# Kernel optimization log

Measured on AMD Instinct MI355X. Metric: run time of the kernel, lower is better.

The kernel has to match this reference:

```python
import jax, jax.numpy as jnp
import numpy as np

B, S, D = 4, 2048, 2048
H, KVH = 16, 4
HD = D // H            # 128
N_REP = H // KVH       # 4
SCALE = HD ** -0.5


def setup_inputs() -> dict:
    key = jax.random.key(0)
    ks = jax.random.split(key, 10)
    w = 0.02
    x = jax.random.normal(ks[0], (B, S, D), jnp.float32)
    # Linear weights stored as [in, out] (y = x @ W + b, equivalent to torch Linear)
    Wq = jax.random.normal(ks[1], (D, D), jnp.float32) * w
    bq = jnp.zeros((D,), jnp.float32)
    Wk = jax.random.normal(ks[2], (D, KVH * HD), jnp.float32) * w
    bk = jnp.zeros((KVH * HD,), jnp.float32)
    Wv = jax.random.normal(ks[3], (D, KVH * HD), jnp.float32) * w
    bv = jnp.zeros((KVH * HD,), jnp.float32)
    Wo = jax.random.normal(ks[4], (D, D), jnp.float32) * w
    bo = jnp.zeros((D,), jnp.float32)
    # RoPE tables: freqs_cis is [max_seq_len, head_dim//2] complex -> cos/sin
    inv_freq = 1.0 / (10000.0 ** (jnp.arange(0, HD, 2, dtype=jnp.float32) / HD))  # [HD//2]
    t = jnp.arange(S, dtype=jnp.float32)
    ang = jnp.outer(t, inv_freq)                     # [S, HD//2]
    freqs_cos = jnp.cos(ang)
    freqs_sin = jnp.sin(ang)
    # causal additive mask [1,1,S,S]
    neg = jnp.float32(-1e9)
    mask = jnp.where(jnp.triu(jnp.ones((S, S), bool), k=1), neg, 0.0)[None, None]
    return {"x": x, "Wq": Wq, "bq": bq, "Wk": Wk, "bk": bk, "Wv": Wv, "bv": bv,
            "Wo": Wo, "bo": bo, "freqs_cos": freqs_cos, "freqs_sin": freqs_sin,
            "mask": mask, "start_pos": 0}


def _apply_rope(q, k, cos, sin):
    # q: [B,S,H,HD], k: [B,S,KVH,HD]; interleaved complex pairs on last dim
    def rot(t):
        tr = t.reshape(*t.shape[:-1], HD // 2, 2)
        xr, xi = tr[..., 0], tr[..., 1]
        c = cos[None, :, None, :]
        s = sin[None, :, None, :]
        yr = xr * c - xi * s
        yi = xr * s + xi * c
        return jnp.stack([yr, yi], axis=-1).reshape(t.shape)
    return rot(q), rot(k)


def reference(x, Wq, bq, Wk, bk, Wv, bv, Wo, bo, freqs_cos, freqs_sin, mask, start_pos):
    Bx, Sx, _ = x.shape
    q = (x @ Wq + bq).reshape(Bx, Sx, H, HD)
    k = (x @ Wk + bk).reshape(Bx, Sx, KVH, HD)
    v = (x @ Wv + bv).reshape(Bx, Sx, KVH, HD)
    q, k = _apply_rope(q, k, freqs_cos, freqs_sin)
    # start_pos = 0 prefill: cache write-then-read is identity, so use k, v directly
    q = q.transpose(0, 2, 1, 3)                      # [B,H,S,HD]
    k = k.transpose(0, 2, 1, 3)                      # [B,KVH,S,HD]
    v = v.transpose(0, 2, 1, 3)
    k = jnp.repeat(k, N_REP, axis=1)                 # repeat_kv -> [B,H,S,HD]
    v = jnp.repeat(v, N_REP, axis=1)
    scores = jnp.einsum("bhsd,bhtd->bhst", q, k) * SCALE + mask
    w = jax.nn.softmax(scores, axis=-1)              # dropout p=0 -> identity
    out = jnp.einsum("bhst,bhtd->bhsd", w, v)
    out = out.transpose(0, 2, 1, 3).reshape(Bx, Sx, D)
    return out @ Wo + bo
```

## Files before the change

kernel.cpp:

```cpp
#include <hip/hip_runtime.h>

typedef unsigned short u16t;
typedef __bf16 bf16x8 __attribute__((ext_vector_type(8)));
typedef float f32x4 __attribute__((ext_vector_type(4)));
typedef float f32x16 __attribute__((ext_vector_type(16)));
typedef unsigned short ushort4_t __attribute__((ext_vector_type(4)));
typedef unsigned short ushort8_t __attribute__((ext_vector_type(8)));

#define B_    4
#define S_    2048
#define D_    2048
#define H_    16
#define KVH_  4
#define HD_   128
#define KDIM  2048
#define SCALE_ 0.08838834764831845f

__device__ __forceinline__ u16t f2bf(float f){
    unsigned u; __builtin_memcpy(&u, &f, 4);
    u += 0x7fffu + ((u >> 16) & 1u);
    return (u16t)(u >> 16);
}
__device__ __forceinline__ void glds16(const u16t* g, u16t* l){
    __builtin_amdgcn_global_load_lds((const __attribute__((address_space(1))) void*)g,
                                     (__attribute__((address_space(3))) void*)l, 16, 0, 0);
}
__device__ __forceinline__ void wg_barrier_lgkm(){
    __builtin_amdgcn_sched_barrier(0);
    asm volatile("s_waitcnt lgkmcnt(0)" ::: "memory");
    __builtin_amdgcn_s_barrier();
    __builtin_amdgcn_sched_barrier(0);
}
__device__ __forceinline__ unsigned cvt_pk_bf16(float lo, float hi){
    unsigned r;
    asm("v_cvt_pk_bf16_f32 %0, %1, %2" : "=v"(r) : "v"(lo), "v"(hi));
    return r;
}
__device__ __forceinline__ void permlane32_swap(unsigned &a, unsigned &b){
    asm volatile("v_permlane32_swap_b32 %0, %1" : "+v"(a), "+v"(b));
}

__global__ void f32_to_bf16(const float* __restrict__ in, u16t* __restrict__ out)
{
    int i = (blockIdx.x * 256 + threadIdx.x) * 4;
    float4 v = *(const float4*)(in + i);
    ushort4_t p;
    p[0] = f2bf(v.x); p[1] = f2bf(v.y); p[2] = f2bf(v.z); p[3] = f2bf(v.w);
    *(ushort4_t*)(out + i) = p;
}

__global__ void transpose_f32_bf16(const float* __restrict__ W, u16t* __restrict__ Wt,
                                   int Ncols, int Krows)
{
    __shared__ u16t tile[32][33];
    int tx = threadIdx.x, ty = threadIdx.y;
    int n = blockIdx.x * 32 + tx, k = blockIdx.y * 32 + ty;
    tile[ty][tx] = f2bf(W[(size_t)k * Ncols + n]);
    __syncthreads();
    int nn = blockIdx.x * 32 + ty, kk = blockIdx.y * 32 + tx;
    Wt[(size_t)nn * Krows + kk] = tile[tx][ty];
}

#define GEMM_PROLOGUE_AND_KLOOP                                                   \
    __shared__ u16t As[128 * 32];                                                 \
    __shared__ u16t Bs[128 * 32];                                                 \
    const int tid  = threadIdx.x;                                                 \
    const int lane = tid & 63, w = tid >> 6;                                      \
    const int wr = (w >> 1) * 64, wc = (w & 1) * 64;                              \
    const int lr = lane & 15, quad = lane >> 4;                                   \
    const int m0 = blockIdx.y * 128, n0 = blockIdx.x * 128;                       \
    f32x4 acc[4][4];                                                              \
    _Pragma("unroll")                                                             \
    for (int r = 0; r < 4; r++)                                                   \
        _Pragma("unroll")                                                         \
        for (int c = 0; c < 4; c++) acc[r][c] = (f32x4){0.f, 0.f, 0.f, 0.f};      \
    for (int k0 = 0; k0 < KDIM; k0 += 32) {                                       \
        __syncthreads();                                                          \
        _Pragma("unroll")                                                         \
        for (int cc = 0; cc < 2; cc++) {                                          \
            int slot = tid + cc * 256;                                            \
            int row = slot >> 2, ko = (slot & 3) * 8;                             \
            glds16(A  + (size_t)(m0 + row) * KDIM + k0 + ko, As + slot * 8);      \
            glds16(Bt + (size_t)(n0 + row) * KDIM + k0 + ko, Bs + slot * 8);      \
        }                                                                         \
        __syncthreads();                                                          \
        bf16x8 a[4], b[4];                                                        \
        _Pragma("unroll")                                                         \
        for (int r = 0; r < 4; r++)                                               \
            a[r] = *(const bf16x8*)(As + (wr + r * 16 + lr) * 32 + quad * 8);     \
        _Pragma("unroll")                                                         \
        for (int c = 0; c < 4; c++)                                               \
            b[c] = *(const bf16x8*)(Bs + (wc + c * 16 + lr) * 32 + quad * 8);     \
        _Pragma("unroll")                                                         \
        for (int r = 0; r < 4; r++)                                               \
            _Pragma("unroll")                                                     \
            for (int c = 0; c < 4; c++)                                           \
                acc[r][c] = __builtin_amdgcn_mfma_f32_16x16x32_bf16(a[r], b[c], acc[r][c], 0, 0, 0); \
    }

__global__ void gemm_o(const u16t* __restrict__ A, const u16t* __restrict__ Bt,
                       const float* __restrict__ bias, float* __restrict__ out)
{
    GEMM_PROLOGUE_AND_KLOOP
#pragma unroll
    for (int r = 0; r < 4; r++) {
#pragma unroll
        for (int c = 0; c < 4; c++) {
            int n = n0 + wc + c * 16 + lr;
            float bval = bias[n];
#pragma unroll
            for (int g = 0; g < 4; g++) {
                int m = m0 + wr + r * 16 + quad * 4 + g;
                out[(size_t)m * D_ + n] = acc[r][c][g] + bval;
            }
        }
    }
}

__global__ void gemm_qkv(const u16t* __restrict__ A, const u16t* __restrict__ Bt,
                         const float* __restrict__ bq, const float* __restrict__ bk,
                         const float* __restrict__ bv,
                         u16t* __restrict__ q_t, u16t* __restrict__ k_t,
                         u16t* __restrict__ v_t,
                         const float* __restrict__ fc, const float* __restrict__ fs)
{
    GEMM_PROLOGUE_AND_KLOOP
    const int region = (blockIdx.x < 16) ? 0 : ((blockIdx.x < 20) ? 1 : 2);
#pragma unroll
    for (int r = 0; r < 4; r++) {
#pragma unroll
        for (int c = 0; c < 4; c++) {
            int n = n0 + wc + c * 16 + lr;
            if (region == 0) {
                float bval = bq[n];
                int hh = n >> 7, d = n & 127, i2 = d >> 1;
#pragma unroll
                for (int g = 0; g < 4; g++) {
                    int m = m0 + wr + r * 16 + quad * 4 + g;
                    int bb = m >> 11, s = m & (S_ - 1);
                    float v = acc[r][c][g] + bval;
                    float p = __shfl_xor(v, 1);
                    float cf = fc[s * 64 + i2], sf = fs[s * 64 + i2];
                    float o = (d & 1) ? (p * sf + v * cf) : (v * cf - p * sf);
                    q_t[(((size_t)bb * H_ + hh) * S_ + s) * HD_ + d] = f2bf(o);
                }
            } else if (region == 1) {
                int nk = n - 2048;
                float bval = bk[nk];
                int hh = nk >> 7, d = nk & 127, i2 = d >> 1;
#pragma unroll
                for (int g = 0; g < 4; g++) {
                    int m = m0 + wr + r * 16 + quad * 4 + g;
                    int bb = m >> 11, s = m & (S_ - 1);
                    float v = acc[r][c][g] + bval;
                    float p = __shfl_xor(v, 1);
                    float cf = fc[s * 64 + i2], sf = fs[s * 64 + i2];
                    float o = (d & 1) ? (p * sf + v * cf) : (v * cf - p * sf);
                    k_t[(((size_t)bb * KVH_ + hh) * S_ + s) * HD_ + d] = f2bf(o);
                }
            } else {
                int nv = n - 2560;
                float bval = bv[nv];
                int kv = nv >> 7, d = nv & 127;
                int mb = m0 + wr + r * 16 + quad * 4;
                int bb = mb >> 11, s = mb & (S_ - 1);
                ushort4_t pk;
#pragma unroll
                for (int g = 0; g < 4; g++) pk[g] = f2bf(acc[r][c][g] + bval);
                *(ushort4_t*)(v_t + (((size_t)bb * KVH_ + kv) * HD_ + d) * S_ + s) = pk;
            }
        }
    }
}

__global__ __launch_bounds__(256, 2) void
attn_kernel(const u16t* __restrict__ qt, const u16t* __restrict__ kt,
            const u16t* __restrict__ vt, u16t* __restrict__ att)
{
    __shared__ char Ks[2][8192];
    __shared__ char Vs[2][8192];
    const int tid  = threadIdx.x;
    const int lane = tid & 63, w = tid >> 6;
    const int l5 = lane & 31, hi = lane >> 5;
    const int bh = blockIdx.y, b = bh >> 4, h = bh & 15, kv = h >> 2;
    const int bx = blockIdx.x;

    const u16t* kb = kt + ((size_t)b * KVH_ + kv) * S_ * HD_;
    const u16t* vb = vt + ((size_t)b * KVH_ + kv) * HD_ * S_;

    f32x16 zero16;
#pragma unroll
    for (int j = 0; j < 16; j++) zero16[j] = 0.f;

    const int krow = tid >> 4, kcol = tid & 15;
    const int vd   = tid >> 2, vcol = tid & 3;
    const int kw0 = ((krow     ) * 256 + kcol * 16) ^ ((krow & 7) << 4);
    const int kw1 = ((krow + 16) * 256 + kcol * 16) ^ ((krow & 7) << 4);
    const int vw0 = ((vd      ) * 64 + vcol * 16) ^ (((vd >> 1) & 3) << 5);
    const int vw1 = ((vd + 64 ) * 64 + vcol * 16) ^ (((vd >> 1) & 3) << 5);

    ushort8_t kr[2][2], vr[2][2];

#pragma unroll 1
    for (int seg = 0; seg < 2; seg++) {
        const int q0 = (seg == 0 ? (15 - bx) : bx) * 128;
        const u16t* qb = qt + (((size_t)b * H_ + h) * S_ + q0) * HD_;

        bf16x8 qa[8];
#pragma unroll
        for (int ks = 0; ks < 8; ks++)
            qa[ks] = *(const bf16x8*)(qb + (w * 32 + l5) * HD_ + ks * 16 + hi * 8);

        f32x16 o[4];
#pragma unroll
        for (int i = 0; i < 4; i++) o[i] = zero16;
        float lpart = 0.f;

        const int ntile = q0 / 32 + 4;
#pragma unroll
        for (int p = 0; p < 2; p++) {
            int t0 = p * 32;
            kr[p][0] = *(const ushort8_t*)(kb + (size_t)(t0 + krow     ) * HD_ + kcol * 8);
            kr[p][1] = *(const ushort8_t*)(kb + (size_t)(t0 + krow + 16) * HD_ + kcol * 8);
            vr[p][0] = *(const ushort8_t*)(vb + (size_t)(vd     ) * S_ + t0 + vcol * 8);
            vr[p][1] = *(const ushort8_t*)(vb + (size_t)(vd + 64) * S_ + t0 + vcol * 8);
        }

        for (int it = 0; it < ntile; it += 2) {
#pragma unroll
            for (int p = 0; p < 2; p++) {
                const int t0 = (it + p) * 32;
                *(ushort8_t*)(Ks[p] + kw0) = kr[p][0];
                *(ushort8_t*)(Ks[p] + kw1) = kr[p][1];
                *(ushort8_t*)(Vs[p] + vw0) = vr[p][0];
                *(ushort8_t*)(Vs[p] + vw1) = vr[p][1];
                const int tn0 = (it + p + 2 < ntile) ? (it + p + 2) * 32 : 0;
                kr[p][0] = *(const ushort8_t*)(kb + (size_t)(tn0 + krow     ) * HD_ + kcol * 8);
                kr[p][1] = *(const ushort8_t*)(kb + (size_t)(tn0 + krow + 16) * HD_ + kcol * 8);
                vr[p][0] = *(const ushort8_t*)(vb + (size_t)(vd     ) * S_ + tn0 + vcol * 8);
                vr[p][1] = *(const ushort8_t*)(vb + (size_t)(vd + 64) * S_ + tn0 + vcol * 8);
                wg_barrier_lgkm();

                if (t0 > q0 + w * 32 + 31) continue;

                f32x16 sa = zero16, sb = zero16;
                __builtin_amdgcn_s_setprio(1);
#pragma unroll
                for (int ks = 0; ks < 8; ks += 2) {
                    bf16x8 kf0 = *(const bf16x8*)(Ks[p] +
                        ((l5 * 256 + ks * 32 + hi * 16) ^ ((l5 & 7) << 4)));
                    sa = __builtin_amdgcn_mfma_f32_32x32x16_bf16(kf0, qa[ks], sa, 0, 0, 0);
                    bf16x8 kf1 = *(const bf16x8*)(Ks[p] +
                        ((l5 * 256 + (ks + 1) * 32 + hi * 16) ^ ((l5 & 7) << 4)));
                    sb = __builtin_amdgcn_mfma_f32_32x32x16_bf16(kf1, qa[ks + 1], sb, 0, 0, 0);
                }
                __builtin_amdgcn_s_setprio(0);
                f32x16 sc = sa + sb;

                float pr[16];
                if (t0 + 31 <= q0 + w * 32) {
#pragma unroll
                    for (int r = 0; r < 16; r++) pr[r] = __expf(sc[r] * SCALE_);
                } else {
                    const int srow = q0 + w * 32 + l5;
#pragma unroll
                    for (int r = 0; r < 16; r++) {
                        int tc = t0 + (r & 3) + 8 * (r >> 2) + 4 * hi;
                        pr[r] = __expf(sc[r] * SCALE_ + ((tc > srow) ? -1e9f : 0.f));
                    }
                }
#pragma unroll
                for (int r = 0; r < 16; r++) lpart += pr[r];

                unsigned d0[4], d1[4];
#pragma unroll
                for (int q4 = 0; q4 < 4; q4++) {
                    d0[q4] = cvt_pk_bf16(pr[4 * q4 + 0], pr[4 * q4 + 1]);
                    d1[q4] = cvt_pk_bf16(pr[4 * q4 + 2], pr[4 * q4 + 3]);
                }
                permlane32_swap(d0[0], d0[1]);
                permlane32_swap(d1[0], d1[1]);
                permlane32_swap(d0[2], d0[3]);
                permlane32_swap(d1[2], d1[3]);
                union { unsigned u[4]; bf16x8 v; } pa0, pa1;
                pa0.u[0] = d0[0]; pa0.u[1] = d1[0]; pa0.u[2] = d0[1]; pa0.u[3] = d1[1];
                pa1.u[0] = d0[2]; pa1.u[1] = d1[2]; pa1.u[2] = d0[3]; pa1.u[3] = d1[3];

                __builtin_amdgcn_s_setprio(1);
#pragma unroll
                for (int dt = 0; dt < 4; dt++) {
                    bf16x8 vf0 = *(const bf16x8*)(Vs[p] +
                        (((dt * 32 + l5) * 64 + hi * 16) ^ (((l5 >> 1) & 3) << 5)));
                    o[dt] = __builtin_amdgcn_mfma_f32_32x32x16_bf16(pa0.v, vf0, o[dt], 0, 0, 0);
                    bf16x8 vf1 = *(const bf16x8*)(Vs[p] +
                        (((dt * 32 + l5) * 64 + 32 + hi * 16) ^ (((l5 >> 1) & 3) << 5)));
                    o[dt] = __builtin_amdgcn_mfma_f32_32x32x16_bf16(pa1.v, vf1, o[dt], 0, 0, 0);
                }
                __builtin_amdgcn_s_setprio(0);
            }
        }

        float lf = lpart + __shfl_xor(lpart, 32);
        float linv = 1.f / lf;
#pragma unroll
        for (int r = 0; r < 16; r++) {
            int qrow = (r & 3) + 8 * (r >> 2) + 4 * hi;
            float iv = __shfl(linv, qrow);
            int s = q0 + w * 32 + qrow;
            u16t* orow = att + ((size_t)(b * S_ + s)) * D_ + h * HD_ + l5;
#pragma unroll
            for (int dt = 0; dt < 4; dt++)
                orow[dt * 32] = f2bf(o[dt][r] * iv);
        }
    }
}

extern "C" void kernel_launch(void* const* d_in, const int* in_sizes, int n_in,
                              void* d_out, int out_size, void* d_ws, size_t ws_size,
                              hipStream_t stream)
{
    const float* x  = (const float*)d_in[0];
    const float* Wq = (const float*)d_in[1];
    const float* bq = (const float*)d_in[2];
    const float* Wk = (const float*)d_in[3];
    const float* bk = (const float*)d_in[4];
    const float* Wv = (const float*)d_in[5];
    const float* bv = (const float*)d_in[6];
    const float* Wo = (const float*)d_in[7];
    const float* bo = (const float*)d_in[8];
    const float* fc = (const float*)d_in[9];
    const float* fs = (const float*)d_in[10];

    const size_t M1 = (size_t)1024 * 1024;
    u16t* ws   = (u16t*)d_ws;
    u16t* x_bf = ws;
    u16t* att  = ws;
    u16t* Wqt  = ws + 16 * M1;
    u16t* Wot  = ws + 16 * M1;
    u16t* Wkt  = ws + 20 * M1;
    u16t* Wvt  = ws + 21 * M1;
    u16t* k_t  = ws + 22 * M1;
    u16t* v_t  = ws + 26 * M1;
    u16t* q_t  = (u16t*)d_out;

    f32_to_bf16<<<dim3(16384), 256, 0, stream>>>(x, x_bf);

    dim3 tb(32, 32);
    transpose_f32_bf16<<<dim3(64, 64), tb, 0, stream>>>(Wq, Wqt, 2048, 2048);
    transpose_f32_bf16<<<dim3(16, 64), tb, 0, stream>>>(Wk, Wkt, 512, 2048);
    transpose_f32_bf16<<<dim3(16, 64), tb, 0, stream>>>(Wv, Wvt, 512, 2048);

    gemm_qkv<<<dim3(24, 64), 256, 0, stream>>>(x_bf, Wqt, bq, bk, bv,
                                               q_t, k_t, v_t, fc, fs);

    attn_kernel<<<dim3(8, 64), 256, 0, stream>>>(q_t, k_t, v_t, att);

    transpose_f32_bf16<<<dim3(64, 64), tb, 0, stream>>>(Wo, Wot, 2048, 2048);

    gemm_o<<<dim3(16, 64), 256, 0, stream>>>(att, Wot, bo, (float*)d_out);
}
```

Baseline: 487.2 us.

## Double K-tile per barrier and remap GEMM workgroups across XCDs

The GEMM K-loop now loads two 32-wide K slices per iteration into separate LDS buffers, halving the number of barrier pairs and doubling the loads in flight per sync. Workgroup IDs are also remapped so that consecutive tiles land on the same XCD (orig&7 round-robin), which is meant to improve L2 reuse of shared A/B rows. The cost is double the LDS footprint, which may reduce occupancy, and the remap assumes the grid size is divisible by 8.

New measurement: 465.0 us. 1.05x faster.

```diff
diff --git a/kernel.cpp b/kernel.cpp
--- a/kernel.cpp
+++ b/kernel.cpp
@@ -61,36 +61,52 @@
     Wt[(size_t)nn * Krows + kk] = tile[tx][ty];
 }
 
-#define GEMM_PROLOGUE_AND_KLOOP                                                   \
-    __shared__ u16t As[128 * 32];                                                 \
-    __shared__ u16t Bs[128 * 32];                                                 \
+#define GEMM_PROLOGUE_AND_KLOOP(GRIDX, NWG)                                       \
+    __shared__ u16t As0[128 * 32], As1[128 * 32];                                 \
+    __shared__ u16t Bs0[128 * 32], Bs1[128 * 32];                                 \
     const int tid  = threadIdx.x;                                                 \
     const int lane = tid & 63, w = tid >> 6;                                      \
     const int wr = (w >> 1) * 64, wc = (w & 1) * 64;                              \
     const int lr = lane & 15, quad = lane >> 4;                                   \
-    const int m0 = blockIdx.y * 128, n0 = blockIdx.x * 128;                       \
+    const int orig = blockIdx.y * (GRIDX) + blockIdx.x;                           \
+    const int lin  = (orig & 7) * ((NWG) / 8) + (orig >> 3);                      \
+    const int bxs  = lin % (GRIDX), bys = lin / (GRIDX);                          \
+    const int m0 = bys * 128, n0 = bxs * 128;                                     \
     f32x4 acc[4][4];                                                              \
     _Pragma("unroll")                                                             \
     for (int r = 0; r < 4; r++)                                                   \
         _Pragma("unroll")                                                         \
         for (int c = 0; c < 4; c++) acc[r][c] = (f32x4){0.f, 0.f, 0.f, 0.f};      \
-    for (int k0 = 0; k0 < KDIM; k0 += 32) {                                       \
+    for (int k0 = 0; k0 < KDIM; k0 += 64) {                                       \
         __syncthreads();                                                          \
         _Pragma("unroll")                                                         \
         for (int cc = 0; cc < 2; cc++) {                                          \
             int slot = tid + cc * 256;                                            \
             int row = slot >> 2, ko = (slot & 3) * 8;                             \
-            glds16(A  + (size_t)(m0 + row) * KDIM + k0 + ko, As + slot * 8);      \
-            glds16(Bt + (size_t)(n0 + row) * KDIM + k0 + ko, Bs + slot * 8);      \
+            glds16(A  + (size_t)(m0 + row) * KDIM + k0 + ko,      As0 + slot * 8);\
+            glds16(A  + (size_t)(m0 + row) * KDIM + k0 + 32 + ko, As1 + slot * 8);\
+            glds16(Bt + (size_t)(n0 + row) * KDIM + k0 + ko,      Bs0 + slot * 8);\
+            glds16(Bt + (size_t)(n0 + row) * KDIM + k0 + 32 + ko, Bs1 + slot * 8);\
         }                                                                         \
         __syncthreads();                                                          \
         bf16x8 a[4], b[4];                                                        \
         _Pragma("unroll")                                                         \
         for (int r = 0; r < 4; r++)                                               \
-            a[r] = *(const bf16x8*)(As + (wr + r * 16 + lr) * 32 + quad * 8);     \
+            a[r] = *(const bf16x8*)(As0 + (wr + r * 16 + lr) * 32 + quad * 8);    \
         _Pragma("unroll")                                                         \
         for (int c = 0; c < 4; c++)                                               \
-            b[c] = *(const bf16x8*)(Bs + (wc + c * 16 + lr) * 32 + quad * 8);     \
+            b[c] = *(const bf16x8*)(Bs0 + (wc + c * 16 + lr) * 32 + quad * 8);    \
+        _Pragma("unroll")                                                         \
+        for (int r = 0; r < 4; r++)                                               \
+            _Pragma("unroll")                                                     \
+            for (int c = 0; c < 4; c++)                                           \
+                acc[r][c] = __builtin_amdgcn_mfma_f32_16x16x32_bf16(a[r], b[c], acc[r][c], 0, 0, 0); \
+        _Pragma("unroll")                                                         \
+        for (int r = 0; r < 4; r++)                                               \
+            a[r] = *(const bf16x8*)(As1 + (wr + r * 16 + lr) * 32 + quad * 8);    \
+        _Pragma("unroll")                                                         \
+        for (int c = 0; c < 4; c++)                                               \
+            b[c] = *(const bf16x8*)(Bs1 + (wc + c * 16 + lr) * 32 + quad * 8);    \
         _Pragma("unroll")                                                         \
         for (int r = 0; r < 4; r++)                                               \
             _Pragma("unroll")                                                     \
@@ -101,7 +117,7 @@
 __global__ void gemm_o(const u16t* __restrict__ A, const u16t* __restrict__ Bt,
                        const float* __restrict__ bias, float* __restrict__ out)
 {
-    GEMM_PROLOGUE_AND_KLOOP
+    GEMM_PROLOGUE_AND_KLOOP(16, 1024)
 #pragma unroll
     for (int r = 0; r < 4; r++) {
 #pragma unroll
@@ -124,8 +140,8 @@
                          u16t* __restrict__ v_t,
                          const float* __restrict__ fc, const float* __restrict__ fs)
 {
-    GEMM_PROLOGUE_AND_KLOOP
-    const int region = (blockIdx.x < 16) ? 0 : ((blockIdx.x < 20) ? 1 : 2);
+    GEMM_PROLOGUE_AND_KLOOP(24, 1536)
+    const int region = (bxs < 16) ? 0 : ((bxs < 20) ? 1 : 2);
 #pragma unroll
     for (int r = 0; r < 4; r++) {
 #pragma unroll
```

## Rewrite GEMMs as 256x256 double-buffered tiles with swizzled LDS and XCD remap

Applied to the files above, without the earlier changes.

Both projection GEMMs move from 128x128 tiles with a 32-wide K step and two syncthreads per step to 256x256 tiles on 512 threads with a 64-wide K step. Global-to-LDS loads are double-buffered and prefetched two stages ahead, waited on with a partial vmcnt barrier. LDS rows use an XOR swizzle to avoid bank conflicts, and block IDs are remapped so neighbouring tiles land on the same XCD. The aim is higher MFMA utilisation and more data reuse, at the cost of 128KB of LDS per block, fewer blocks in flight (384 and 256), and more register pressure.

After: 483.1 us. No clear change (-0.8%).

```diff
diff --git a/kernel.cpp b/kernel.cpp
--- a/kernel.cpp
+++ b/kernel.cpp
@@ -31,6 +31,12 @@
     __builtin_amdgcn_s_barrier();
     __builtin_amdgcn_sched_barrier(0);
 }
+__device__ __forceinline__ void wg_barrier_vm8(){
+    __builtin_amdgcn_sched_barrier(0);
+    asm volatile("s_waitcnt vmcnt(8)" ::: "memory");
+    __builtin_amdgcn_s_barrier();
+    __builtin_amdgcn_sched_barrier(0);
+}
 __device__ __forceinline__ unsigned cvt_pk_bf16(float lo, float hi){
     unsigned r;
     asm("v_cvt_pk_bf16_f32 %0, %1, %2" : "=v"(r) : "v"(lo), "v"(hi));
@@ -61,82 +67,129 @@
     Wt[(size_t)nn * Krows + kk] = tile[tx][ty];
 }
 
-#define GEMM_PROLOGUE_AND_KLOOP                                                   \
-    __shared__ u16t As[128 * 32];                                                 \
-    __shared__ u16t Bs[128 * 32];                                                 \
+#define GEMM256_PROLOGUE_AND_KLOOP(GRIDX, NWG)                                    \
+    __shared__ u16t As[2][256 * 64];                                              \
+    __shared__ u16t Bs[2][256 * 64];                                              \
     const int tid  = threadIdx.x;                                                 \
-    const int lane = tid & 63, w = tid >> 6;                                      \
-    const int wr = (w >> 1) * 64, wc = (w & 1) * 64;                              \
+    const int lane = tid & 63, w = tid >> 6;                       \
+    const int wm = w >> 2, wn = w & 3;                                            \
     const int lr = lane & 15, quad = lane >> 4;                                   \
-    const int m0 = blockIdx.y * 128, n0 = blockIdx.x * 128;                       \
-    f32x4 acc[4][4];                                                              \
+    const int sx = (lr & 7) << 4;                                                 \
+    const int orig = blockIdx.y * (GRIDX) + blockIdx.x;                           \
+    const int lin  = (orig & 7) * ((NWG) / 8) + (orig >> 3);                      \
+    const int bxs  = lin % (GRIDX), bys = lin / (GRIDX);                          \
+    const int m0 = bys * 256, n0 = bxs * 256;                                     \
+           \
+    const int rw = w * 8 + (lane >> 3);                       \
+    const int ce = ((lane & 7) ^ (lane >> 3)) * 8;          \
+    f32x4 acc[8][4];                                                              \
     _Pragma("unroll")                                                             \
-    for (int r = 0; r < 4; r++)                                                   \
+    for (int r = 0; r < 8; r++)                                                   \
         _Pragma("unroll")                                                         \
         for (int c = 0; c < 4; c++) acc[r][c] = (f32x4){0.f, 0.f, 0.f, 0.f};      \
-    for (int k0 = 0; k0 < KDIM; k0 += 32) {                                       \
-        __syncthreads();                                                          \
+                 \
+    _Pragma("unroll")                                                             \
+    for (int j = 0; j < 4; j++) {                                                 \
+        glds16(A  + (size_t)(m0 + j * 64 + rw) * KDIM + ce,                       \
+               &As[0][(j * 8 + w) * 512 + lane * 8]);                             \
+        glds16(Bt + (size_t)(n0 + j * 64 + rw) * KDIM + ce,                       \
+               &Bs[0][(j * 8 + w) * 512 + lane * 8]);                             \
+    }                                                                             \
+    _Pragma("unroll")                                                             \
+    for (int j = 0; j < 4; j++) {                                                 \
+        glds16(A  + (size_t)(m0 + j * 64 + rw) * KDIM + 64 + ce,                  \
+               &As[1][(j * 8 + w) * 512 + lane * 8]);                             \
+        glds16(Bt + (size_t)(n0 + j * 64 + rw) * KDIM + 64 + ce,                  \
+               &Bs[1][(j * 8 + w) * 512 + lane * 8]);                             \
+    }                                                                             \
+    wg_barrier_vm8();                                                             \
+    _Pragma("unroll 1")                                                           \
+    for (int t = 0; t < KDIM / 64; t++) {                                         \
+        const int p = t & 1;                                                      \
+        const char* Ab = (const char*)&As[p][0];                                  \
+        const char* Bb = (const char*)&Bs[p][0];                                  \
+        bf16x8 bfr[4][2];                                                         \
         _Pragma("unroll")                                                         \
-        for (int cc = 0; cc < 2; cc++) {                                          \
-            int slot = tid + cc * 256;                                            \
-            int row = slot >> 2, ko = (slot & 3) * 8;                             \
-            glds16(A  + (size_t)(m0 + row) * KDIM + k0 + ko, As + slot * 8);      \
-            glds16(Bt + (size_t)(n0 + row) * KDIM + k0 + ko, Bs + slot * 8);      \
+        for (int c = 0; c < 4; c++) {                                             \
+            int Rb = (wn * 64 + c * 16 + lr) * 128;                               \
+            bfr[c][0] = *(const bf16x8*)(Bb + ((Rb + quad * 16) ^ sx));           \
+            bfr[c][1] = *(const bf16x8*)(Bb + ((Rb + 64 + quad * 16) ^ sx));      \
         }                                                                         \
-        __syncthreads();                                                          \
-        bf16x8 a[4], b[4];                                                        \
         _Pragma("unroll")                                                         \
-        for (int r = 0; r < 4; r++)                                               \
-            a[r] = *(const bf16x8*)(As + (wr + r * 16 + lr) * 32 + quad * 8);     \
+        for (int half = 0; half < 2; half++) {                                    \
+            bf16x8 afr[4][2];                                                     \
+            _Pragma("unroll")                                                     \
+            for (int r = 0; r < 4; r++) {                                         \
+                int Ra = (wm * 128 + (half * 4 + r) * 16 + lr) * 128;             \
+                afr[r][0] = *(const bf16x8*)(Ab + ((Ra + quad * 16) ^ sx));       \
+                afr[r][1] = *(const bf16x8*)(Ab + ((Ra + 64 + quad * 16) ^ sx));  \
+            }                                                                     \
+            __builtin_amdgcn_s_setprio(1);                                        \
+            _Pragma("unroll")                                                     \
+            for (int r = 0; r < 4; r++)                                           \
+                _Pragma("unroll")                                                 \
+                for (int c = 0; c < 4; c++) {                                     \
+                    acc[half*4+r][c] = __builtin_amdgcn_mfma_f32_16x16x32_bf16(   \
+                        afr[r][0], bfr[c][0], acc[half*4+r][c], 0, 0, 0);         \
+                    acc[half*4+r][c] = __builtin_amdgcn_mfma_f32_16x16x32_bf16(   \
+                        afr[r][1], bfr[c][1], acc[half*4+r][c], 0, 0, 0);         \
+                }                                                                 \
+            __builtin_amdgcn_s_setprio(0);                                        \
+        }                                                                         \
+        wg_barrier_lgkm();                       \
+        const int tn = (t + 2 < KDIM / 64) ? (t + 2) : 0;     \
+        const int kn = tn * 64;                                                   \
         _Pragma("unroll")                                                         \
-        for (int c = 0; c < 4; c++)                                               \
-            b[c] = *(const bf16x8*)(Bs + (wc + c * 16 + lr) * 32 + quad * 8);     \
-        _Pragma("unroll")                                                         \
-        for (int r = 0; r < 4; r++)                                               \
-            _Pragma("unroll")                                                     \
-            for (int c = 0; c < 4; c++)                                           \
-                acc[r][c] = __builtin_amdgcn_mfma_f32_16x16x32_bf16(a[r], b[c], acc[r][c], 0, 0, 0); \
+        for (int j = 0; j < 4; j++) {                                             \
+            glds16(A  + (size_t)(m0 + j * 64 + rw) * KDIM + kn + ce,              \
+                   &As[p][(j * 8 + w) * 512 + lane * 8]);                         \
+            glds16(Bt + (size_t)(n0 + j * 64 + rw) * KDIM + kn + ce,              \
+                   &Bs[p][(j * 8 + w) * 512 + lane * 8]);                         \
+        }                                                                         \
+        wg_barrier_vm8();                   \
     }
 
-__global__ void gemm_o(const u16t* __restrict__ A, const u16t* __restrict__ Bt,
-                       const float* __restrict__ bias, float* __restrict__ out)
-{
-    GEMM_PROLOGUE_AND_KLOOP
-#pragma unroll
-    for (int r = 0; r < 4; r++) {
+__global__ __launch_bounds__(512, 2) void
+gemm_o(const u16t* __restrict__ A, const u16t* __restrict__ Bt,
+       const float* __restrict__ bias, float* __restrict__ out)
+{
+    GEMM256_PROLOGUE_AND_KLOOP(8, 256)
+#pragma unroll
+    for (int r = 0; r < 8; r++) {
 #pragma unroll
         for (int c = 0; c < 4; c++) {
-            int n = n0 + wc + c * 16 + lr;
+            int n = n0 + wn * 64 + c * 16 + lr;
             float bval = bias[n];
 #pragma unroll
             for (int g = 0; g < 4; g++) {
-                int m = m0 + wr + r * 16 + quad * 4 + g;
+                int m = m0 + wm * 128 + r * 16 + quad * 4 + g;
                 out[(size_t)m * D_ + n] = acc[r][c][g] + bval;
             }
         }
     }
 }
 
-__global__ void gemm_qkv(const u16t* __restrict__ A, const u16t* __restrict__ Bt,
-                         const float* __restrict__ bq, const float* __restrict__ bk,
-                         const float* __restrict__ bv,
-                         u16t* __restrict__ q_t, u16t* __restrict__ k_t,
-                         u16t* __restrict__ v_t,
-                         const float* __restrict__ fc, const float* __restrict__ fs)
-{
-    GEMM_PROLOGUE_AND_KLOOP
-    const int region = (blockIdx.x < 16) ? 0 : ((blockIdx.x < 20) ? 1 : 2);
-#pragma unroll
-    for (int r = 0; r < 4; r++) {
+__global__ __launch_bounds__(512, 2) void
+gemm_qkv(const u16t* __restrict__ A, const u16t* __restrict__ Bt,
+         const float* __restrict__ bq, const float* __restrict__ bk,
+         const float* __restrict__ bv,
+         u16t* __restrict__ q_t, u16t* __restrict__ k_t,
+         u16t* __restrict__ v_t,
+         const float* __restrict__ fc, const float* __restrict__ fs)
+{
+    GEMM256_PROLOGUE_AND_KLOOP(12, 384)
+    const int region = (bxs < 8) ? 0 : ((bxs < 10) ? 1 : 2);
+#pragma unroll
+    for (int r = 0; r < 8; r++) {
 #pragma unroll
         for (int c = 0; c < 4; c++) {
-            int n = n0 + wc + c * 16 + lr;
+            int n = n0 + wn * 64 + c * 16 + lr;
             if (region == 0) {
                 float bval = bq[n];
                 int hh = n >> 7, d = n & 127, i2 = d >> 1;
 #pragma unroll
                 for (int g = 0; g < 4; g++) {
-                    int m = m0 + wr + r * 16 + quad * 4 + g;
+                    int m = m0 + wm * 128 + r * 16 + quad * 4 + g;
                     int bb = m >> 11, s = m & (S_ - 1);
                     float v = acc[r][c][g] + bval;
                     float p = __shfl_xor(v, 1);
@@ -150,7 +203,7 @@
                 int hh = nk >> 7, d = nk & 127, i2 = d >> 1;
 #pragma unroll
                 for (int g = 0; g < 4; g++) {
-                    int m = m0 + wr + r * 16 + quad * 4 + g;
+                    int m = m0 + wm * 128 + r * 16 + quad * 4 + g;
                     int bb = m >> 11, s = m & (S_ - 1);
                     float v = acc[r][c][g] + bval;
                     float p = __shfl_xor(v, 1);
@@ -162,7 +215,7 @@
                 int nv = n - 2560;
                 float bval = bv[nv];
                 int kv = nv >> 7, d = nv & 127;
-                int mb = m0 + wr + r * 16 + quad * 4;
+                int mb = m0 + wm * 128 + r * 16 + quad * 4;
                 int bb = mb >> 11, s = mb & (S_ - 1);
                 ushort4_t pk;
 #pragma unroll
@@ -350,12 +403,12 @@
     transpose_f32_bf16<<<dim3(16, 64), tb, 0, stream>>>(Wk, Wkt, 512, 2048);
     transpose_f32_bf16<<<dim3(16, 64), tb, 0, stream>>>(Wv, Wvt, 512, 2048);
 
-    gemm_qkv<<<dim3(24, 64), 256, 0, stream>>>(x_bf, Wqt, bq, bk, bv,
+    gemm_qkv<<<dim3(12, 32), 512, 0, stream>>>(x_bf, Wqt, bq, bk, bv,
                                                q_t, k_t, v_t, fc, fs);
 
     attn_kernel<<<dim3(8, 64), 256, 0, stream>>>(q_t, k_t, v_t, att);
 
     transpose_f32_bf16<<<dim3(64, 64), tb, 0, stream>>>(Wo, Wot, 2048, 2048);
 
-    gemm_o<<<dim3(16, 64), 256, 0, stream>>>(att, Wot, bo, (float*)d_out);
-}
+    gemm_o<<<dim3(8, 32), 512, 0, stream>>>(att, Wot, bo, (float*)d_out);
+}
```

## Double-buffer GEMM K-loop with swizzled LDS and grouped block remap

Applied to the files above, without the earlier changes.

The QKV and output-projection GEMMs now use a double-buffered LDS pipeline with a K-tile of 64: the next tile is prefetched via global_load_lds while MFMAs consume the current one, leaving one barrier per iteration instead of two. LDS reads use an XOR swizzle to avoid bank conflicts, block indices are remapped in groups of 8 for better L2 reuse, and MFMA sections raise wave priority. The cost is doubled LDS use per block (64 KB), which may reduce occupancy. A variable in the attention kernel is renamed to avoid a clash with the new macro.

Measured after the change: 465.9 us. -4.4%, faster.

```diff
diff --git a/kernel.cpp b/kernel.cpp
--- a/kernel.cpp
+++ b/kernel.cpp
@@ -31,6 +31,12 @@
     __builtin_amdgcn_s_barrier();
     __builtin_amdgcn_sched_barrier(0);
 }
+__device__ __forceinline__ void wg_barrier_vm0(){
+    __builtin_amdgcn_sched_barrier(0);
+    asm volatile("s_waitcnt vmcnt(0)" ::: "memory");
+    __builtin_amdgcn_s_barrier();
+    __builtin_amdgcn_sched_barrier(0);
+}
 __device__ __forceinline__ unsigned cvt_pk_bf16(float lo, float hi){
     unsigned r;
     asm("v_cvt_pk_bf16_f32 %0, %1, %2" : "=v"(r) : "v"(lo), "v"(hi));
@@ -61,47 +67,79 @@
     Wt[(size_t)nn * Krows + kk] = tile[tx][ty];
 }
 
-#define GEMM_PROLOGUE_AND_KLOOP                                                   \
-    __shared__ u16t As[128 * 32];                                                 \
-    __shared__ u16t Bs[128 * 32];                                                 \
+#define GEMM128_CORE(GRIDX, NWG)                                                  \
+    __shared__ u16t As[2][128 * 64];                                              \
+    __shared__ u16t Bs[2][128 * 64];                                              \
     const int tid  = threadIdx.x;                                                 \
     const int lane = tid & 63, w = tid >> 6;                                      \
     const int wr = (w >> 1) * 64, wc = (w & 1) * 64;                              \
     const int lr = lane & 15, quad = lane >> 4;                                   \
-    const int m0 = blockIdx.y * 128, n0 = blockIdx.x * 128;                       \
+    const int sxr = lr & 7;                           \
+    const int orig = blockIdx.y * (GRIDX) + blockIdx.x;                           \
+    const int lin  = (orig & 7) * ((NWG) / 8) + (orig >> 3);                      \
+    const int bxs  = lin % (GRIDX), bys = lin / (GRIDX);                          \
+    const int m0 = bys * 128, n0 = bxs * 128;                                     \
+        \
+         \
+    const int srow = tid >> 3;                                                    \
+    const int sko  = (((tid & 7) ^ ((tid >> 3) & 7)) << 3);                       \
     f32x4 acc[4][4];                                                              \
     _Pragma("unroll")                                                             \
     for (int r = 0; r < 4; r++)                                                   \
         _Pragma("unroll")                                                         \
         for (int c = 0; c < 4; c++) acc[r][c] = (f32x4){0.f, 0.f, 0.f, 0.f};      \
-    for (int k0 = 0; k0 < KDIM; k0 += 32) {                                       \
-        __syncthreads();                                                          \
+    _Pragma("unroll")                                                             \
+    for (int j = 0; j < 4; j++) {                                                 \
+        glds16(A  + (size_t)(m0 + j * 32 + srow) * KDIM + sko,                    \
+               &As[0][(j * 256 + tid) * 8]);                                      \
+        glds16(Bt + (size_t)(n0 + j * 32 + srow) * KDIM + sko,                    \
+               &Bs[0][(j * 256 + tid) * 8]);                                      \
+    }                                                                             \
+    wg_barrier_vm0();                                                             \
+    _Pragma("unroll 1")                                                           \
+    for (int t = 0; t < KDIM / 64; t++) {                                         \
+        const int p = t & 1;                                                      \
+        const int kn = ((t + 1 < KDIM / 64) ? (t + 1) : (KDIM / 64 - 1)) * 64;    \
         _Pragma("unroll")                                                         \
-        for (int cc = 0; cc < 2; cc++) {                                          \
-            int slot = tid + cc * 256;                                            \
-            int row = slot >> 2, ko = (slot & 3) * 8;                             \
-            glds16(A  + (size_t)(m0 + row) * KDIM + k0 + ko, As + slot * 8);      \
-            glds16(Bt + (size_t)(n0 + row) * KDIM + k0 + ko, Bs + slot * 8);      \
+        for (int j = 0; j < 4; j++) {                                             \
+            glds16(A  + (size_t)(m0 + j * 32 + srow) * KDIM + kn + sko,           \
+                   &As[p ^ 1][(j * 256 + tid) * 8]);                              \
+            glds16(Bt + (size_t)(n0 + j * 32 + srow) * KDIM + kn + sko,           \
+                   &Bs[p ^ 1][(j * 256 + tid) * 8]);                              \
         }                                                                         \
-        __syncthreads();                                                          \
-        bf16x8 a[4], b[4];                                                        \
+        __builtin_amdgcn_sched_barrier(0);                                        \
         _Pragma("unroll")                                                         \
-        for (int r = 0; r < 4; r++)                                               \
-            a[r] = *(const bf16x8*)(As + (wr + r * 16 + lr) * 32 + quad * 8);     \
-        _Pragma("unroll")                                                         \
-        for (int c = 0; c < 4; c++)                                               \
-            b[c] = *(const bf16x8*)(Bs + (wc + c * 16 + lr) * 32 + quad * 8);     \
-        _Pragma("unroll")                                                         \
-        for (int r = 0; r < 4; r++)                                               \
+        for (int half = 0; half < 2; half++) {                                    \
+            bf16x8 a[4], b[4];                                                    \
             _Pragma("unroll")                                                     \
-            for (int c = 0; c < 4; c++)                                           \
-                acc[r][c] = __builtin_amdgcn_mfma_f32_16x16x32_bf16(a[r], b[c], acc[r][c], 0, 0, 0); \
+            for (int r = 0; r < 4; r++) {                                         \
+                int row = wr + r * 16 + lr;                                       \
+                a[r] = *(const bf16x8*)(&As[p][row * 64 +                         \
+                          (((half * 4 + quad) ^ sxr) << 3)]);                     \
+            }                                                                     \
+            _Pragma("unroll")                                                     \
+            for (int c = 0; c < 4; c++) {                                         \
+                int row = wc + c * 16 + lr;                                       \
+                b[c] = *(const bf16x8*)(&Bs[p][row * 64 +                         \
+                          (((half * 4 + quad) ^ sxr) << 3)]);                     \
+            }                                                                     \
+            __builtin_amdgcn_s_setprio(1);                                        \
+            _Pragma("unroll")                                                     \
+            for (int r = 0; r < 4; r++)                                           \
+                _Pragma("unroll")                                                 \
+                for (int c = 0; c < 4; c++)                                       \
+                    acc[r][c] = __builtin_amdgcn_mfma_f32_16x16x32_bf16(          \
+                        a[r], b[c], acc[r][c], 0, 0, 0);                          \
+            __builtin_amdgcn_s_setprio(0);                                        \
+        }                                                                         \
+        wg_barrier_vm0();                                                         \
     }
 
-__global__ void gemm_o(const u16t* __restrict__ A, const u16t* __restrict__ Bt,
-                       const float* __restrict__ bias, float* __restrict__ out)
-{
-    GEMM_PROLOGUE_AND_KLOOP
+__global__ __launch_bounds__(256) void
+gemm_o(const u16t* __restrict__ A, const u16t* __restrict__ Bt,
+       const float* __restrict__ bias, float* __restrict__ out)
+{
+    GEMM128_CORE(16, 1024)
 #pragma unroll
     for (int r = 0; r < 4; r++) {
 #pragma unroll
@@ -117,15 +155,16 @@
     }
 }
 
-__global__ void gemm_qkv(const u16t* __restrict__ A, const u16t* __restrict__ Bt,
-                         const float* __restrict__ bq, const float* __restrict__ bk,
-                         const float* __restrict__ bv,
-                         u16t* __restrict__ q_t, u16t* __restrict__ k_t,
-                         u16t* __restrict__ v_t,
-                         const float* __restrict__ fc, const float* __restrict__ fs)
-{
-    GEMM_PROLOGUE_AND_KLOOP
-    const int region = (blockIdx.x < 16) ? 0 : ((blockIdx.x < 20) ? 1 : 2);
+__global__ __launch_bounds__(256) void
+gemm_qkv(const u16t* __restrict__ A, const u16t* __restrict__ Bt,
+         const float* __restrict__ bq, const float* __restrict__ bk,
+         const float* __restrict__ bv,
+         u16t* __restrict__ q_t, u16t* __restrict__ k_t,
+         u16t* __restrict__ v_t,
+         const float* __restrict__ fc, const float* __restrict__ fs)
+{
+    GEMM128_CORE(24, 1536)
+    const int region = (bxs < 16) ? 0 : ((bxs < 20) ? 1 : 2);
 #pragma unroll
     for (int r = 0; r < 4; r++) {
 #pragma unroll
@@ -262,11 +301,11 @@
 #pragma unroll
                     for (int r = 0; r < 16; r++) pr[r] = __expf(sc[r] * SCALE_);
                 } else {
-                    const int srow = q0 + w * 32 + l5;
+                    const int srow2 = q0 + w * 32 + l5;
 #pragma unroll
                     for (int r = 0; r < 16; r++) {
                         int tc = t0 + (r & 3) + 8 * (r >> 2) + 4 * hi;
-                        pr[r] = __expf(sc[r] * SCALE_ + ((tc > srow) ? -1e9f : 0.f));
+                        pr[r] = __expf(sc[r] * SCALE_ + ((tc > srow2) ? -1e9f : 0.f));
                     }
                 }
 #pragma unroll
```
